# Optimization experiments

Measured on AMD Instinct MI355X. Metric: run time of the kernel, lower is better.

## Reference

```python
import jax, jax.numpy as jnp
import numpy as np

# dims (match init_kwargs / input_specs)
B, T, IN, H, OUT, BR = 128, 250, 700, 512, 20, 4
VTH, DT, WARMUP = 1.0, 1.0, 10


@jax.custom_vjp
def spike_fn(v):
    # Heaviside spike with surrogate gradient (ActFun_adp style)
    return (v > 0.0).astype(v.dtype)

def _spike_fwd(v):
    return spike_fn(v), v

def _spike_bwd(v, g):
    gamma, lens = 0.5, 0.5  # gaussian surrogate
    return (g * gamma * jnp.exp(-v * v / (2.0 * lens * lens)),)

spike_fn.defvjp(_spike_fwd, _spike_bwd)


def make_mask(rng, out_dim, in_dim, branch):
    # each output neuron's branch j sees a disjoint random slice of inputs
    m = np.zeros((out_dim * branch, in_dim), np.float32)
    seg = in_dim // branch
    for i in range(out_dim):
        perm = rng.permutation(in_dim)
        for j in range(branch):
            m[i * branch + j, perm[j * seg:(j + 1) * seg]] = 1.0
    return jnp.asarray(m)


def setup_inputs() -> dict:
    key = jax.random.key(0)
    ks = jax.random.split(key, 12)
    rng = np.random.default_rng(0)
    lim1 = 1.0 / np.sqrt(IN)
    lim2 = 1.0 / np.sqrt(H)
    return {
        "x": jax.random.uniform(ks[0], (B, T, IN), dtype=jnp.float32),
        "W1": jax.random.uniform(ks[1], (H * BR, IN), minval=-lim1, maxval=lim1),
        "b1": jax.random.uniform(ks[2], (H * BR,), minval=-lim1, maxval=lim1),
        "tau_m1": jax.random.uniform(ks[3], (H,), minval=0.0, maxval=4.0),
        "tau_n1": jax.random.uniform(ks[4], (H, BR), minval=0.0, maxval=4.0),
        "mask1": make_mask(rng, H, IN, BR),
        "W2": jax.random.uniform(ks[5], (H * BR, H), minval=-lim2, maxval=lim2),
        "b2": jax.random.uniform(ks[6], (H * BR,), minval=-lim2, maxval=lim2),
        "tau_m2": jax.random.uniform(ks[7], (H,), minval=0.0, maxval=4.0),
        "tau_n2": jax.random.uniform(ks[8], (H, BR), minval=0.0, maxval=4.0),
        "mask2": make_mask(rng, H, H, BR),
        "Wo": jax.random.uniform(ks[9], (OUT, H), minval=-lim2, maxval=lim2),
        "bo": jax.random.uniform(ks[10], (OUT,), minval=-lim2, maxval=lim2),
        "tau_mo": jax.random.uniform(ks[11], (OUT,), minval=0.0, maxval=4.0),
    }


def reference(x, W1, b1, tau_m1, tau_n1, mask1, W2, b2, tau_m2, tau_n2, mask2, Wo, bo, tau_mo):
    beta1 = jax.nn.sigmoid(tau_n1)   # [H,BR] dendritic decay
    alpha1 = jax.nn.sigmoid(tau_m1)  # [H]   membrane decay
    beta2 = jax.nn.sigmoid(tau_n2)
    alpha2 = jax.nn.sigmoid(tau_m2)
    alpha_o = jax.nn.sigmoid(tau_mo)  # [OUT]
    Wm1 = W1 * mask1  # dendritic branch connectivity mask
    Wm2 = W2 * mask2
    Bsz = x.shape[0]
    Hd, Br = tau_n1.shape
    Od = tau_mo.shape[0]

    init = (jnp.zeros((Bsz, Hd, Br)), jnp.zeros((Bsz, Hd)), jnp.zeros((Bsz, Hd)),
            jnp.zeros((Bsz, Hd, Br)), jnp.zeros((Bsz, Hd)), jnp.zeros((Bsz, Hd)),
            jnp.zeros((Bsz, Od)))

    def step(c, xt):
        d1, m1, s1, d2, m2, s2, mo = c
        # layer 1: dendritic filter then LIF membrane with soft reset
        d1 = beta1 * d1 + (1.0 - beta1) * (xt @ Wm1.T + b1).reshape(Bsz, Hd, Br)
        m1 = m1 * alpha1 + (1.0 - alpha1) * DT * d1.sum(-1) - VTH * s1
        s1 = spike_fn(m1 - VTH)
        # layer 2
        d2 = beta2 * d2 + (1.0 - beta2) * (s1 @ Wm2.T + b2).reshape(Bsz, Hd, Br)
        m2 = m2 * alpha2 + (1.0 - alpha2) * DT * d2.sum(-1) - VTH * s2
        s2 = spike_fn(m2 - VTH)
        # leaky readout integrator (no spiking)
        mo = mo * alpha_o + (1.0 - alpha_o) * DT * (s2 @ Wo.T + bo)
        return (d1, m1, s1, d2, m2, s2, mo), jax.nn.softmax(mo, axis=1)

    _, ys = jax.lax.scan(step, init, jnp.swapaxes(x, 0, 1))  # ys: [T,B,OUT]
    # readout_mode == 'sum_softmax': skip steps i <= warmup_steps, sum the rest
    return ys[WARMUP + 1:].sum(0)
```

## Files before the change

kernel.cpp:

```cpp
#include <hip/hip_runtime.h>
#include <math.h>
#include <stdint.h>

#define B_    128
#define T_    250
#define IN_   700
#define INP_  704
#define H_    512
#define OUT_  20
#define BR_   4
#define HB_   2048
#define WARM_ 10
#define VTH_  1.0f

typedef __attribute__((ext_vector_type(8)))  _Float16 half8;
typedef __attribute__((ext_vector_type(4)))  float f32x4;
typedef __attribute__((ext_vector_type(16))) float f32x16;
typedef __attribute__((ext_vector_type(4)))  int i32x4;
typedef __attribute__((ext_vector_type(16))) int i32x16;
typedef const __attribute__((address_space(1))) void* gptr_t;
typedef __attribute__((address_space(3))) void* lptr_t;

__global__ __launch_bounds__(256)
void w1prep_kernel(const float* __restrict__ W, const float* __restrict__ M,
                   _Float16* __restrict__ w0, _Float16* __restrict__ w1) {
    int i = blockIdx.x * 256 + threadIdx.x;
    if (i >= HB_ * INP_) return;
    int r = i / INP_, c = i - r * INP_;
    float v = (c < IN_) ? W[(size_t)r * IN_ + c] * M[(size_t)r * IN_ + c] : 0.f;
    _Float16 h0 = (_Float16)v;
    w0[i] = h0;
    w1[i] = (_Float16)(v - (float)h0);
}

__global__ __launch_bounds__(256)
void w2prep_kernel(const float* __restrict__ W, const float* __restrict__ M,
                   int8_t* __restrict__ p2, int8_t* __restrict__ p1,
                   int8_t* __restrict__ p0) {
    int i = blockIdx.x * 256 + threadIdx.x;
    if (i >= HB_ * H_) return;
    float v = W[i] * M[i];
    int q = (int)lrintf(v * 67108864.f);
    int b0 = (int)(int8_t)(q & 0xFF);  q = (q - b0) >> 8;
    int b1 = (int)(int8_t)(q & 0xFF);  int b2 = (q - b1) >> 8;
    p0[i] = (int8_t)b0; p1[i] = (int8_t)b1; p2[i] = (int8_t)b2;
}

__global__ __launch_bounds__(256)
void woprep_kernel(const float* __restrict__ Wo, _Float16* __restrict__ wo0,
                   _Float16* __restrict__ wo1) {
    int i = blockIdx.x * 256 + threadIdx.x;
    if (i >= 32 * H_) return;
    int n = i >> 9;
    float v = (n < OUT_) ? Wo[(size_t)n * H_ + (i & (H_ - 1))] : 0.f;
    _Float16 h0 = (_Float16)v;
    wo0[i] = h0;
    wo1[i] = (_Float16)(v - (float)h0);
}

__global__ __launch_bounds__(256)
void convx_kernel(const float* __restrict__ x, _Float16* __restrict__ x0,
                  _Float16* __restrict__ x1, int t0, int tc, int ntot) {
    int i = blockIdx.x * 256 + threadIdx.x;
    if (i >= ntot) return;
    int r = i / INP_, c = i - r * INP_;
    int bb = r / tc, tl = r - bb * tc;
    float v = (c < IN_) ? x[((size_t)bb * T_ + t0 + tl) * IN_ + c] : 0.f;
    _Float16 h0 = (_Float16)v;
    x0[i] = h0;
    x1[i] = (_Float16)(v - (float)h0);
}

__global__ void zero_kernel(float* __restrict__ p, int n4) {
    int i = blockIdx.x * blockDim.x + threadIdx.x;
    if (i < n4) ((float4*)p)[i] = make_float4(0.f, 0.f, 0.f, 0.f);
}

__global__ __launch_bounds__(256)
void l1_gemm_kernel(const _Float16* __restrict__ x0, const _Float16* __restrict__ x1,
                    const _Float16* __restrict__ w0, const _Float16* __restrict__ w1,
                    const float* __restrict__ bias, float* __restrict__ C) {
    __shared__ alignas(16) _Float16 A0s[128 * 32];
    __shared__ alignas(16) _Float16 A1s[128 * 32];
    __shared__ alignas(16) _Float16 B0s[128 * 32];
    __shared__ alignas(16) _Float16 B1s[128 * 32];
    const int tid  = threadIdx.x;
    const int wave = tid >> 6, lane = tid & 63;
    const int bm = blockIdx.y * 128, bn = blockIdx.x * 128;

    const int    srow  = tid >> 2;
    const int    skoff = (((tid & 3) ^ ((srow >> 1) & 3)) * 8);
    const size_t aoff0 = (size_t)(bm + srow) * INP_ + skoff;
    const size_t aoff1 = aoff0 + (size_t)64 * INP_;
    const size_t boff0 = (size_t)(bn + srow) * INP_ + skoff;
    const size_t boff1 = boff0 + (size_t)64 * INP_;
    const int lo0 = wave * 512, lo1 = 2048 + wave * 512;

    const int wm = wave & 1, wn = wave >> 1;
    const int row = lane & 31;
    const int khq = lane >> 5;
    const int key = (lane >> 1) & 3;
    const int cK0 = ((0 + khq) ^ key) * 8;
    const int cK1 = ((2 + khq) ^ key) * 8;

    f32x16 acc[2][2] = {};

    for (int kt = 0; kt < INP_ / 32; kt++) {
        const int k0 = kt * 32;
        __builtin_amdgcn_global_load_lds((gptr_t)(x0 + aoff0 + k0), (lptr_t)(A0s + lo0), 16, 0, 0);
        __builtin_amdgcn_global_load_lds((gptr_t)(x0 + aoff1 + k0), (lptr_t)(A0s + lo1), 16, 0, 0);
        __builtin_amdgcn_global_load_lds((gptr_t)(x1 + aoff0 + k0), (lptr_t)(A1s + lo0), 16, 0, 0);
        __builtin_amdgcn_global_load_lds((gptr_t)(x1 + aoff1 + k0), (lptr_t)(A1s + lo1), 16, 0, 0);
        __builtin_amdgcn_global_load_lds((gptr_t)(w0 + boff0 + k0), (lptr_t)(B0s + lo0), 16, 0, 0);
        __builtin_amdgcn_global_load_lds((gptr_t)(w0 + boff1 + k0), (lptr_t)(B0s + lo1), 16, 0, 0);
        __builtin_amdgcn_global_load_lds((gptr_t)(w1 + boff0 + k0), (lptr_t)(B1s + lo0), 16, 0, 0);
        __builtin_amdgcn_global_load_lds((gptr_t)(w1 + boff1 + k0), (lptr_t)(B1s + lo1), 16, 0, 0);
        __syncthreads();

        half8 a0f[2][2], a1f[2][2], b0f[2][2], b1f[2][2];
#pragma unroll
        for (int mt = 0; mt < 2; mt++) {
            const _Float16* ar = &A0s[(wm * 64 + mt * 32 + row) * 32];
            a0f[mt][0] = *(const half8*)&ar[cK0];
            a0f[mt][1] = *(const half8*)&ar[cK1];
        }
#pragma unroll
        for (int nt = 0; nt < 2; nt++) {
            const _Float16* br = &B0s[(wn * 64 + nt * 32 + row) * 32];
            b0f[nt][0] = *(const half8*)&br[cK0];
            b0f[nt][1] = *(const half8*)&br[cK1];
        }
#pragma unroll
        for (int ks = 0; ks < 2; ks++)
#pragma unroll
            for (int mt = 0; mt < 2; mt++)
#pragma unroll
                for (int nt = 0; nt < 2; nt++)
                    acc[mt][nt] = __builtin_amdgcn_mfma_f32_32x32x16_f16(
                        a0f[mt][ks], b0f[nt][ks], acc[mt][nt], 0, 0, 0);
#pragma unroll
        for (int nt = 0; nt < 2; nt++) {
            const _Float16* br = &B1s[(wn * 64 + nt * 32 + row) * 32];
            b1f[nt][0] = *(const half8*)&br[cK0];
            b1f[nt][1] = *(const half8*)&br[cK1];
        }
#pragma unroll
        for (int ks = 0; ks < 2; ks++)
#pragma unroll
            for (int mt = 0; mt < 2; mt++)
#pragma unroll
                for (int nt = 0; nt < 2; nt++)
                    acc[mt][nt] = __builtin_amdgcn_mfma_f32_32x32x16_f16(
                        a0f[mt][ks], b1f[nt][ks], acc[mt][nt], 0, 0, 0);
#pragma unroll
        for (int mt = 0; mt < 2; mt++) {
            const _Float16* ar = &A1s[(wm * 64 + mt * 32 + row) * 32];
            a1f[mt][0] = *(const half8*)&ar[cK0];
            a1f[mt][1] = *(const half8*)&ar[cK1];
        }
#pragma unroll
        for (int ks = 0; ks < 2; ks++)
#pragma unroll
            for (int mt = 0; mt < 2; mt++)
#pragma unroll
                for (int nt = 0; nt < 2; nt++)
                    acc[mt][nt] = __builtin_amdgcn_mfma_f32_32x32x16_f16(
                        a1f[mt][ks], b0f[nt][ks], acc[mt][nt], 0, 0, 0);
        __syncthreads();
    }

    const int col = lane & 31;
    const int rb  = 4 * (lane >> 5);
#pragma unroll
    for (int nt = 0; nt < 2; nt++) {
        const int gc = bn + wn * 64 + nt * 32 + col;
        const float bv = bias[gc];
#pragma unroll
        for (int mt = 0; mt < 2; mt++) {
#pragma unroll
            for (int reg = 0; reg < 16; reg++) {
                const int gr = bm + wm * 64 + mt * 32 + (reg & 3) + 8 * (reg >> 2) + rb;
                C[(size_t)gr * HB_ + gc] = acc[mt][nt][reg] + bv;
            }
        }
    }
}

__global__ __launch_bounds__(256)
void mfma_i8_gemm_kernel(const int8_t* __restrict__ A,
                         const int8_t* __restrict__ p2, const int8_t* __restrict__ p1,
                         const int8_t* __restrict__ p0,
                         const float* __restrict__ bias, float* __restrict__ C) {
    __shared__ alignas(16) int8_t As[128 * 64];
    __shared__ alignas(16) int8_t Bs[128 * 64];
    const int tid  = threadIdx.x;
    const int wave = tid >> 6, lane = tid & 63;
    const int bm = blockIdx.y * 128, bn = blockIdx.x * 128;

    const int    srow  = tid >> 2;
    const int    skoff = (((tid & 3) ^ ((srow >> 1) & 3)) * 16);
    const size_t aoff0 = (size_t)(bm + srow) * H_ + skoff;
    const size_t aoff1 = aoff0 + (size_t)64 * H_;
    const size_t boff0 = (size_t)(bn + srow) * H_ + skoff;
    const size_t boff1 = boff0 + (size_t)64 * H_;
    lptr_t lA0 = (lptr_t)(As + wave * 1024);
    lptr_t lA1 = (lptr_t)(As + 4096 + wave * 1024);
    lptr_t lB0 = (lptr_t)(Bs + wave * 1024);
    lptr_t lB1 = (lptr_t)(Bs + 4096 + wave * 1024);

    const int wm = wave & 1, wn = wave >> 1;
    const int row = lane & 31;
    const int khq = lane >> 5;
    const int key = (lane >> 1) & 3;
    const int cK0 = ((0 + khq) ^ key) * 16;
    const int cK1 = ((2 + khq) ^ key) * 16;

    const int8_t* planes[3] = {p2, p1, p0};
    i32x16 acc[2][2] = {};

#pragma unroll
    for (int s = 0; s < 3; s++) {
        if (s) {
#pragma unroll
            for (int mt = 0; mt < 2; mt++)
#pragma unroll
                for (int nt = 0; nt < 2; nt++) acc[mt][nt] *= 256;
        }
        const int8_t* pw = planes[s];
        for (int kt = 0; kt < H_ / 64; kt++) {
            const int k0 = kt * 64;
            __builtin_amdgcn_global_load_lds((gptr_t)(A  + aoff0 + k0), lA0, 16, 0, 0);
            __builtin_amdgcn_global_load_lds((gptr_t)(A  + aoff1 + k0), lA1, 16, 0, 0);
            __builtin_amdgcn_global_load_lds((gptr_t)(pw + boff0 + k0), lB0, 16, 0, 0);
            __builtin_amdgcn_global_load_lds((gptr_t)(pw + boff1 + k0), lB1, 16, 0, 0);
            __syncthreads();

            i32x4 af[2][2], bf[2][2];
#pragma unroll
            for (int mt = 0; mt < 2; mt++) {
                const int8_t* ar = &As[(wm * 64 + mt * 32 + row) * 64];
                af[mt][0] = *(const i32x4*)&ar[cK0];
                af[mt][1] = *(const i32x4*)&ar[cK1];
            }
#pragma unroll
            for (int nt = 0; nt < 2; nt++) {
                const int8_t* br = &Bs[(wn * 64 + nt * 32 + row) * 64];
                bf[nt][0] = *(const i32x4*)&br[cK0];
                bf[nt][1] = *(const i32x4*)&br[cK1];
            }
#pragma unroll
            for (int ks = 0; ks < 2; ks++)
#pragma unroll
                for (int mt = 0; mt < 2; mt++)
#pragma unroll
                    for (int nt = 0; nt < 2; nt++)
                        acc[mt][nt] = __builtin_amdgcn_mfma_i32_32x32x32_i8(
                            af[mt][ks], bf[nt][ks], acc[mt][nt], 0, 0, 0);
            __syncthreads();
        }
    }

    const float scale = 1.f / 67108864.f;
    const int col = lane & 31;
    const int rb  = 4 * (lane >> 5);
#pragma unroll
    for (int nt = 0; nt < 2; nt++) {
        const int gc = bn + wn * 64 + nt * 32 + col;
        const float bv = bias[gc];
#pragma unroll
        for (int mt = 0; mt < 2; mt++) {
#pragma unroll
            for (int reg = 0; reg < 16; reg++) {
                const int gr = bm + wm * 64 + mt * 32 + (reg & 3) + 8 * (reg >> 2) + rb;
                C[(size_t)gr * HB_ + gc] = (float)acc[mt][nt][reg] * scale + bv;
            }
        }
    }
}

#define SCAN_BODY(SPIKE_STORE)                                                  \
    int idx = blockIdx.x * 256 + threadIdx.x;                                   \
    int b = idx >> 9;                                                           \
    int h = idx & (H_ - 1);                                                     \
    float alpha = 1.f / (1.f + expf(-tau_m[h]));                                \
    float4 tn = ((const float4*)tau_n)[h];                                      \
    float4 beta;                                                                \
    beta.x = 1.f / (1.f + expf(-tn.x));                                         \
    beta.y = 1.f / (1.f + expf(-tn.y));                                         \
    beta.z = 1.f / (1.f + expf(-tn.z));                                         \
    beta.w = 1.f / (1.f + expf(-tn.w));                                         \
    float4 d = ((const float4*)dst)[idx];                                       \
    float m = mst[idx];                                                         \
    float sp = spst[idx];                                                       \
    const float* cp = cur + (size_t)b * tc * HB_ + h * BR_;                     \
    for (int t = 0; t < tc; t++) {                                              \
        float4 c = *(const float4*)cp;                                          \
        cp += HB_;                                                              \
        d.x = beta.x * d.x + (1.f - beta.x) * c.x;                              \
        d.y = beta.y * d.y + (1.f - beta.y) * c.y;                              \
        d.z = beta.z * d.z + (1.f - beta.z) * c.z;                              \
        d.w = beta.w * d.w + (1.f - beta.w) * c.w;                              \
        float s4 = ((d.x + d.y) + d.z) + d.w;                                   \
        m = m * alpha + (1.f - alpha) * s4 - VTH_ * sp;                         \
        sp = (m > VTH_) ? 1.f : 0.f;                                            \
        SPIKE_STORE;                                                            \
    }                                                                           \
    ((float4*)dst)[idx] = d;                                                    \
    mst[idx] = m;                                                               \
    spst[idx] = sp;

__global__ __launch_bounds__(256)
void scan_i8_kernel(const float* __restrict__ cur, float* __restrict__ dst,
                    float* __restrict__ mst, float* __restrict__ spst,
                    int8_t* __restrict__ sout, const float* __restrict__ tau_m,
                    const float* __restrict__ tau_n, int tc) {
    SCAN_BODY(sout[((size_t)b * tc + t) * H_ + h] = (int8_t)(m > VTH_))
}

__global__ __launch_bounds__(256)
void scan_f16_kernel(const float* __restrict__ cur, float* __restrict__ dst,
                     float* __restrict__ mst, float* __restrict__ spst,
                     _Float16* __restrict__ sout, const float* __restrict__ tau_m,
                     const float* __restrict__ tau_n, int tc) {
    SCAN_BODY(sout[((size_t)b * tc + t) * H_ + h] = (_Float16)sp)
}

__global__ __launch_bounds__(256)
void rdot_mfma_kernel(const _Float16* __restrict__ s2c, const _Float16* __restrict__ wo0,
                      const _Float16* __restrict__ wo1, const float* __restrict__ bo,
                      float* __restrict__ curo, int t0, int tc) {
    __shared__ alignas(16) _Float16 As[128 * 32];
    __shared__ alignas(16) _Float16 B0s[32 * 32];
    __shared__ alignas(16) _Float16 B1s[32 * 32];
    const int tid  = threadIdx.x;
    const int wave = tid >> 6, lane = tid & 63;
    const int bm = blockIdx.x * 128;

    const int    srow  = tid >> 2;
    const int    skoff = (((tid & 3) ^ ((srow >> 1) & 3)) * 8);
    const size_t aoff0 = (size_t)(bm + srow) * H_ + skoff;
    const size_t aoff1 = aoff0 + (size_t)64 * H_;
    lptr_t lA0 = (lptr_t)(As + wave * 512);
    lptr_t lA1 = (lptr_t)(As + 2048 + wave * 512);
    const _Float16* bsrc = (wave < 2) ? wo0 : wo1;
    const int bw = wave & 1;
    const size_t boff = (size_t)(bw * 16 + (lane >> 2)) * H_
                      + ((lane & 3) ^ ((lane >> 3) & 3)) * 8;
    lptr_t lB = (lptr_t)(((wave < 2) ? B0s : B1s) + bw * 512);

    const int fr = lane & 15;
    const int key = (lane >> 1) & 3;
    const int cK  = (((lane >> 4) ^ key) * 8);

    f32x4 acc[2][2] = {};

    for (int kt = 0; kt < H_ / 32; kt++) {
        const int k0 = kt * 32;
        __builtin_amdgcn_global_load_lds((gptr_t)(s2c + aoff0 + k0), lA0, 16, 0, 0);
        __builtin_amdgcn_global_load_lds((gptr_t)(s2c + aoff1 + k0), lA1, 16, 0, 0);
        __builtin_amdgcn_global_load_lds((gptr_t)(bsrc + boff + k0), lB, 16, 0, 0);
        __syncthreads();

        half8 af[2], b0[2], b1[2];
#pragma unroll
        for (int mi = 0; mi < 2; mi++)
            af[mi] = *(const half8*)&As[(wave * 32 + mi * 16 + fr) * 32 + cK];
#pragma unroll
        for (int ni = 0; ni < 2; ni++) {
            b0[ni] = *(const half8*)&B0s[(ni * 16 + fr) * 32 + cK];
            b1[ni] = *(const half8*)&B1s[(ni * 16 + fr) * 32 + cK];
        }
#pragma unroll
        for (int mi = 0; mi < 2; mi++)
#pragma unroll
            for (int ni = 0; ni < 2; ni++) {
                acc[mi][ni] = __builtin_amdgcn_mfma_f32_16x16x32_f16(af[mi], b0[ni], acc[mi][ni], 0, 0, 0);
                acc[mi][ni] = __builtin_amdgcn_mfma_f32_16x16x32_f16(af[mi], b1[ni], acc[mi][ni], 0, 0, 0);
            }
        __syncthreads();
    }

    const int cc = lane & 15;
    const int cr = (lane >> 4) * 4;
#pragma unroll
    for (int ni = 0; ni < 2; ni++) {
        const int gc = ni * 16 + cc;
        if (gc < OUT_) {
            const float bv = bo[gc];
#pragma unroll
            for (int mi = 0; mi < 2; mi++) {
#pragma unroll
                for (int r = 0; r < 4; r++) {
                    const int gr = bm + wave * 32 + mi * 16 + cr + r;
                    const int bb = gr / tc, tl = gr - bb * tc;
                    curo[((size_t)bb * T_ + t0 + tl) * OUT_ + gc] = acc[mi][ni][r] + bv;
                }
            }
        }
    }
}

#define RT_SEG 12
#define RT_LEN 21

__global__ __launch_bounds__(256)
void readout_kernel(const float* __restrict__ curo, const float* __restrict__ tau_mo,
                    float* __restrict__ out) {
    __shared__ float moS[T_ * OUT_];
    __shared__ float segA[RT_SEG][OUT_];
    __shared__ float segU[RT_SEG][OUT_];
    __shared__ float pre[RT_SEG][OUT_];
    __shared__ float accS[OUT_];
    const int b = blockIdx.x;
    const int tid = threadIdx.x;
    const float* cb = curo + (size_t)b * T_ * OUT_;

    const int o = tid % OUT_;
    const int sg = tid / OUT_;
    const float ao = 1.f / (1.f + expf(-tau_mo[o]));

    if (tid < RT_SEG * OUT_) {
        int t0 = sg * RT_LEN;
        int t1 = min(T_, t0 + RT_LEN);
        float u = 0.f, Ap = 1.f;
        for (int t = t0; t < t1; t++) {
            u = ao * u + (1.f - ao) * cb[t * OUT_ + o];
            Ap *= ao;
        }
        segU[sg][o] = u; segA[sg][o] = Ap;
    }
    if (tid < OUT_) accS[tid] = 0.f;
    __syncthreads();
    if (tid < OUT_) {
        float m = 0.f;
        for (int s = 0; s < RT_SEG; s++) {
            pre[s][tid] = m;
            m = segA[s][tid] * m + segU[s][tid];
        }
    }
    __syncthreads();
    if (tid < RT_SEG * OUT_) {
        int t0 = sg * RT_LEN;
        int t1 = min(T_, t0 + RT_LEN);
        float m = pre[sg][o];
        for (int t = t0; t < t1; t++) {
            m = ao * m + (1.f - ao) * cb[t * OUT_ + o];
            moS[t * OUT_ + o] = m;
        }
    }
    __syncthreads();
    if (tid >= WARM_ + 1 && tid < T_) {
        int t = tid;
        float mx = -3.0e38f;
#pragma unroll
        for (int o2 = 0; o2 < OUT_; o2++) mx = fmaxf(mx, moS[t * OUT_ + o2]);
        float es[OUT_]; float se = 0.f;
#pragma unroll
        for (int o2 = 0; o2 < OUT_; o2++) {
            float e = expf(moS[t * OUT_ + o2] - mx);
            es[o2] = e; se += e;
        }
        float inv = 1.f / se;
#pragma unroll
        for (int o2 = 0; o2 < OUT_; o2++) atomicAdd(&accS[o2], es[o2] * inv);
    }
    __syncthreads();
    if (tid < OUT_) out[(size_t)b * OUT_ + tid] = accS[tid];
}

extern "C" void kernel_launch(void* const* d_in, const int* in_sizes, int n_in,
                              void* d_out, int out_size, void* d_ws, size_t ws_size,
                              hipStream_t stream) {
    const float* x      = (const float*)d_in[0];
    const float* W1     = (const float*)d_in[1];
    const float* b1     = (const float*)d_in[2];
    const float* tau_m1 = (const float*)d_in[3];
    const float* tau_n1 = (const float*)d_in[4];
    const float* mask1  = (const float*)d_in[5];
    const float* W2     = (const float*)d_in[6];
    const float* b2     = (const float*)d_in[7];
    const float* tau_m2 = (const float*)d_in[8];
    const float* tau_n2 = (const float*)d_in[9];
    const float* mask2  = (const float*)d_in[10];
    const float* Wo     = (const float*)d_in[11];
    const float* bo     = (const float*)d_in[12];
    const float* tau_mo = (const float*)d_in[13];
    float* out = (float*)d_out;

    int ncs;  int tcs[3];
    bool single = (ws_size >= (size_t)368000000);
    if (single)                                { ncs = 1; tcs[0] = 250; }
    else if (ws_size >= (size_t)219000000)     { ncs = 2; tcs[0] = tcs[1] = 125; }
    else                                       { ncs = 3; tcs[0] = 100; tcs[1] = 100; tcs[2] = 50; }
    const int tcm = tcs[0];

    char* p = (char*)d_ws;
    auto alloc = [&](size_t bytes) { char* r = p; p += (bytes + 255) & ~(size_t)255; return r; };
    _Float16* w10 = (_Float16*)alloc((size_t)HB_ * INP_ * 2);
    _Float16* w11 = (_Float16*)alloc((size_t)HB_ * INP_ * 2);
    int8_t*   q2  = (int8_t*)alloc((size_t)HB_ * H_);
    int8_t*   q1  = (int8_t*)alloc((size_t)HB_ * H_);
    int8_t*   q0  = (int8_t*)alloc((size_t)HB_ * H_);
    _Float16* wo0 = (_Float16*)alloc((size_t)32 * H_ * 2);
    _Float16* wo1 = (_Float16*)alloc((size_t)32 * H_ * 2);
    _Float16* xc0 = (_Float16*)alloc((size_t)B_ * tcm * INP_ * 2);
    _Float16* xc1 = (_Float16*)alloc((size_t)B_ * tcm * INP_ * 2);
    int8_t*   s1c;
    _Float16* s2c;
    if (single) {
        s1c = (int8_t*)xc0;
        s2c = (_Float16*)xc1;
    } else {
        s1c = (int8_t*)alloc((size_t)B_ * tcm * H_);
        s2c = (_Float16*)alloc((size_t)B_ * tcm * H_ * 2);
    }
    float* cur    = (float*)alloc((size_t)B_ * tcm * HB_ * 4);
    float* curo   = (float*)alloc((size_t)B_ * T_ * OUT_ * 4);
    float* st     = (float*)alloc((size_t)786432 * 4);
    float* d1  = st;
    float* m1  = d1 + (size_t)B_ * H_ * BR_;
    float* sp1 = m1 + (size_t)B_ * H_;
    float* d2  = sp1 + (size_t)B_ * H_;
    float* m2  = d2 + (size_t)B_ * H_ * BR_;
    float* sp2 = m2 + (size_t)B_ * H_;

    w1prep_kernel<<<(HB_ * INP_ + 255) / 256, 256, 0, stream>>>(W1, mask1, w10, w11);
    w2prep_kernel<<<(HB_ * H_ + 255) / 256, 256, 0, stream>>>(W2, mask2, q2, q1, q0);
    woprep_kernel<<<(32 * H_ + 255) / 256, 256, 0, stream>>>(Wo, wo0, wo1);
    zero_kernel<<<(786432 / 4 + 255) / 256, 256, 0, stream>>>(st, 786432 / 4);

    int t0 = 0;
    for (int c = 0; c < ncs; c++) {
        const int tc = tcs[c];
        const int M = B_ * tc;
        dim3 gg(HB_ / 128, M / 128);
        convx_kernel<<<(M * INP_ + 255) / 256, 256, 0, stream>>>(x, xc0, xc1, t0, tc, M * INP_);
        l1_gemm_kernel<<<gg, 256, 0, stream>>>(xc0, xc1, w10, w11, b1, cur);
        scan_i8_kernel<<<B_ * H_ / 256, 256, 0, stream>>>(cur, d1, m1, sp1, s1c, tau_m1, tau_n1, tc);
        mfma_i8_gemm_kernel<<<gg, 256, 0, stream>>>(s1c, q2, q1, q0, b2, cur);
        scan_f16_kernel<<<B_ * H_ / 256, 256, 0, stream>>>(cur, d2, m2, sp2, s2c, tau_m2, tau_n2, tc);
        rdot_mfma_kernel<<<M / 128, 256, 0, stream>>>(s2c, wo0, wo1, bo, curo, t0, tc);
        t0 += tc;
    }
    readout_kernel<<<B_, 256, 0, stream>>>(curo, tau_mo, out);
}
```

Before: 826.3 us.

## Double-buffer LDS in GEMM kernels to overlap global loads with MFMA

Converts the layer-1 split-f16 GEMM, the int8 bit-plane GEMM and the readout MFMA kernel to double-buffered LDS staging. The next K tile is prefetched with global_load_lds while the current tile is computed, and one barrier per iteration replaces two. The int8 kernel's three plane loops are flattened into a single 24-step pipelined loop, with the accumulator rescaled at the plane boundaries. s_setprio is raised around the MFMA blocks. LDS use per block doubles, which may lower occupancy.

```diff
diff --git a/kernel.cpp b/kernel.cpp
--- a/kernel.cpp
+++ b/kernel.cpp
@@ -80,10 +80,7 @@
 void l1_gemm_kernel(const _Float16* __restrict__ x0, const _Float16* __restrict__ x1,
                     const _Float16* __restrict__ w0, const _Float16* __restrict__ w1,
                     const float* __restrict__ bias, float* __restrict__ C) {
-    __shared__ alignas(16) _Float16 A0s[128 * 32];
-    __shared__ alignas(16) _Float16 A1s[128 * 32];
-    __shared__ alignas(16) _Float16 B0s[128 * 32];
-    __shared__ alignas(16) _Float16 B1s[128 * 32];
+    __shared__ alignas(16) _Float16 S[2 * 16384];
     const int tid  = threadIdx.x;
     const int wave = tid >> 6, lane = tid & 63;
     const int bm = blockIdx.y * 128, bn = blockIdx.x * 128;
@@ -94,7 +91,7 @@
     const size_t aoff1 = aoff0 + (size_t)64 * INP_;
     const size_t boff0 = (size_t)(bn + srow) * INP_ + skoff;
     const size_t boff1 = boff0 + (size_t)64 * INP_;
-    const int lo0 = wave * 512, lo1 = 2048 + wave * 512;
+    const int lo = wave * 512;
 
     const int wm = wave & 1, wn = wave >> 1;
     const int row = lane & 31;
@@ -105,31 +102,38 @@
 
     f32x16 acc[2][2] = {};
 
-    for (int kt = 0; kt < INP_ / 32; kt++) {
+    auto stage = [&](int kt, int base) {
         const int k0 = kt * 32;
-        __builtin_amdgcn_global_load_lds((gptr_t)(x0 + aoff0 + k0), (lptr_t)(A0s + lo0), 16, 0, 0);
-        __builtin_amdgcn_global_load_lds((gptr_t)(x0 + aoff1 + k0), (lptr_t)(A0s + lo1), 16, 0, 0);
-        __builtin_amdgcn_global_load_lds((gptr_t)(x1 + aoff0 + k0), (lptr_t)(A1s + lo0), 16, 0, 0);
-        __builtin_amdgcn_global_load_lds((gptr_t)(x1 + aoff1 + k0), (lptr_t)(A1s + lo1), 16, 0, 0);
-        __builtin_amdgcn_global_load_lds((gptr_t)(w0 + boff0 + k0), (lptr_t)(B0s + lo0), 16, 0, 0);
-        __builtin_amdgcn_global_load_lds((gptr_t)(w0 + boff1 + k0), (lptr_t)(B0s + lo1), 16, 0, 0);
-        __builtin_amdgcn_global_load_lds((gptr_t)(w1 + boff0 + k0), (lptr_t)(B1s + lo0), 16, 0, 0);
-        __builtin_amdgcn_global_load_lds((gptr_t)(w1 + boff1 + k0), (lptr_t)(B1s + lo1), 16, 0, 0);
-        __syncthreads();
-
+        _Float16* Sb = S + base;
+        __builtin_amdgcn_global_load_lds((gptr_t)(x0 + aoff0 + k0), (lptr_t)(Sb + lo),          16, 0, 0);
+        __builtin_amdgcn_global_load_lds((gptr_t)(x0 + aoff1 + k0), (lptr_t)(Sb + 2048  + lo),  16, 0, 0);
+        __builtin_amdgcn_global_load_lds((gptr_t)(x1 + aoff0 + k0), (lptr_t)(Sb + 4096  + lo),  16, 0, 0);
+        __builtin_amdgcn_global_load_lds((gptr_t)(x1 + aoff1 + k0), (lptr_t)(Sb + 6144  + lo),  16, 0, 0);
+        __builtin_amdgcn_global_load_lds((gptr_t)(w0 + boff0 + k0), (lptr_t)(Sb + 8192  + lo),  16, 0, 0);
+        __builtin_amdgcn_global_load_lds((gptr_t)(w0 + boff1 + k0), (lptr_t)(Sb + 10240 + lo),  16, 0, 0);
+        __builtin_amdgcn_global_load_lds((gptr_t)(w1 + boff0 + k0), (lptr_t)(Sb + 12288 + lo),  16, 0, 0);
+        __builtin_amdgcn_global_load_lds((gptr_t)(w1 + boff1 + k0), (lptr_t)(Sb + 14336 + lo),  16, 0, 0);
+    };
+
+    auto compute = [&](int base) {
+        const _Float16* A0b = S + base;
+        const _Float16* A1b = A0b + 4096;
+        const _Float16* B0b = A0b + 8192;
+        const _Float16* B1b = A0b + 12288;
         half8 a0f[2][2], a1f[2][2], b0f[2][2], b1f[2][2];
 #pragma unroll
         for (int mt = 0; mt < 2; mt++) {
-            const _Float16* ar = &A0s[(wm * 64 + mt * 32 + row) * 32];
+            const _Float16* ar = &A0b[(wm * 64 + mt * 32 + row) * 32];
             a0f[mt][0] = *(const half8*)&ar[cK0];
             a0f[mt][1] = *(const half8*)&ar[cK1];
         }
 #pragma unroll
         for (int nt = 0; nt < 2; nt++) {
-            const _Float16* br = &B0s[(wn * 64 + nt * 32 + row) * 32];
+            const _Float16* br = &B0b[(wn * 64 + nt * 32 + row) * 32];
             b0f[nt][0] = *(const half8*)&br[cK0];
             b0f[nt][1] = *(const half8*)&br[cK1];
         }
+        __builtin_amdgcn_s_setprio(1);
 #pragma unroll
         for (int ks = 0; ks < 2; ks++)
 #pragma unroll
@@ -138,12 +142,14 @@
                 for (int nt = 0; nt < 2; nt++)
                     acc[mt][nt] = __builtin_amdgcn_mfma_f32_32x32x16_f16(
                         a0f[mt][ks], b0f[nt][ks], acc[mt][nt], 0, 0, 0);
+        __builtin_amdgcn_s_setprio(0);
 #pragma unroll
         for (int nt = 0; nt < 2; nt++) {
-            const _Float16* br = &B1s[(wn * 64 + nt * 32 + row) * 32];
+            const _Float16* br = &B1b[(wn * 64 + nt * 32 + row) * 32];
             b1f[nt][0] = *(const half8*)&br[cK0];
             b1f[nt][1] = *(const half8*)&br[cK1];
         }
+        __builtin_amdgcn_s_setprio(1);
 #pragma unroll
         for (int ks = 0; ks < 2; ks++)
 #pragma unroll
@@ -152,12 +158,14 @@
                 for (int nt = 0; nt < 2; nt++)
                     acc[mt][nt] = __builtin_amdgcn_mfma_f32_32x32x16_f16(
                         a0f[mt][ks], b1f[nt][ks], acc[mt][nt], 0, 0, 0);
+        __builtin_amdgcn_s_setprio(0);
 #pragma unroll
         for (int mt = 0; mt < 2; mt++) {
-            const _Float16* ar = &A1s[(wm * 64 + mt * 32 + row) * 32];
+            const _Float16* ar = &A1b[(wm * 64 + mt * 32 + row) * 32];
             a1f[mt][0] = *(const half8*)&ar[cK0];
             a1f[mt][1] = *(const half8*)&ar[cK1];
         }
+        __builtin_amdgcn_s_setprio(1);
 #pragma unroll
         for (int ks = 0; ks < 2; ks++)
 #pragma unroll
@@ -166,8 +174,23 @@
                 for (int nt = 0; nt < 2; nt++)
                     acc[mt][nt] = __builtin_amdgcn_mfma_f32_32x32x16_f16(
                         a1f[mt][ks], b0f[nt][ks], acc[mt][nt], 0, 0, 0);
-        __syncthreads();
-    }
+        __builtin_amdgcn_s_setprio(0);
+    };
+
+    stage(0, 0);
+    asm volatile("s_waitcnt vmcnt(0)" ::: "memory");
+    __builtin_amdgcn_s_barrier();
+
+    int cur = 0;
+    for (int kt = 0; kt < INP_ / 32 - 1; kt++) {
+        const int base = cur * 16384;
+        stage(kt + 1, base ^ 16384);
+        compute(base);
+        asm volatile("s_waitcnt vmcnt(0) lgkmcnt(0)" ::: "memory");
+        __builtin_amdgcn_s_barrier();
+        cur ^= 1;
+    }
+    compute(cur * 16384);
 
     const int col = lane & 31;
     const int rb  = 4 * (lane >> 5);
@@ -191,8 +214,7 @@
                          const int8_t* __restrict__ p2, const int8_t* __restrict__ p1,
                          const int8_t* __restrict__ p0,
                          const float* __restrict__ bias, float* __restrict__ C) {
-    __shared__ alignas(16) int8_t As[128 * 64];
-    __shared__ alignas(16) int8_t Bs[128 * 64];
+    __shared__ alignas(16) int8_t S[2 * 16384];
     const int tid  = threadIdx.x;
     const int wave = tid >> 6, lane = tid & 63;
     const int bm = blockIdx.y * 128, bn = blockIdx.x * 128;
@@ -203,10 +225,7 @@
     const size_t aoff1 = aoff0 + (size_t)64 * H_;
     const size_t boff0 = (size_t)(bn + srow) * H_ + skoff;
     const size_t boff1 = boff0 + (size_t)64 * H_;
-    lptr_t lA0 = (lptr_t)(As + wave * 1024);
-    lptr_t lA1 = (lptr_t)(As + 4096 + wave * 1024);
-    lptr_t lB0 = (lptr_t)(Bs + wave * 1024);
-    lptr_t lB1 = (lptr_t)(Bs + 4096 + wave * 1024);
+    const int lo = wave * 1024;
 
     const int wm = wave & 1, wn = wave >> 1;
     const int row = lane & 31;
@@ -215,50 +234,67 @@
     const int cK0 = ((0 + khq) ^ key) * 16;
     const int cK1 = ((2 + khq) ^ key) * 16;
 
-    const int8_t* planes[3] = {p2, p1, p0};
     i32x16 acc[2][2] = {};
 
-#pragma unroll
-    for (int s = 0; s < 3; s++) {
-        if (s) {
+    auto stage = [&](int i, int base) {
+        const int s  = i >> 3;
+        const int k0 = (i & 7) * 64;
+        const int8_t* pw = (s == 0) ? p2 : (s == 1) ? p1 : p0;
+        int8_t* Sb = S + base;
+        __builtin_amdgcn_global_load_lds((gptr_t)(A  + aoff0 + k0), (lptr_t)(Sb + lo),          16, 0, 0);
+        __builtin_amdgcn_global_load_lds((gptr_t)(A  + aoff1 + k0), (lptr_t)(Sb + 4096  + lo),  16, 0, 0);
+        __builtin_amdgcn_global_load_lds((gptr_t)(pw + boff0 + k0), (lptr_t)(Sb + 8192  + lo),  16, 0, 0);
+        __builtin_amdgcn_global_load_lds((gptr_t)(pw + boff1 + k0), (lptr_t)(Sb + 12288 + lo),  16, 0, 0);
+    };
+
+    auto compute = [&](int base) {
+        const int8_t* Ab = S + base;
+        const int8_t* Bb = Ab + 8192;
+        i32x4 af[2][2], bf[2][2];
+#pragma unroll
+        for (int mt = 0; mt < 2; mt++) {
+            const int8_t* ar = &Ab[(wm * 64 + mt * 32 + row) * 64];
+            af[mt][0] = *(const i32x4*)&ar[cK0];
+            af[mt][1] = *(const i32x4*)&ar[cK1];
+        }
+#pragma unroll
+        for (int nt = 0; nt < 2; nt++) {
+            const int8_t* br = &Bb[(wn * 64 + nt * 32 + row) * 64];
+            bf[nt][0] = *(const i32x4*)&br[cK0];
+            bf[nt][1] = *(const i32x4*)&br[cK1];
+        }
+        __builtin_amdgcn_s_setprio(1);
+#pragma unroll
+        for (int ks = 0; ks < 2; ks++)
 #pragma unroll
             for (int mt = 0; mt < 2; mt++)
 #pragma unroll
+                for (int nt = 0; nt < 2; nt++)
+                    acc[mt][nt] = __builtin_amdgcn_mfma_i32_32x32x32_i8(
+                        af[mt][ks], bf[nt][ks], acc[mt][nt], 0, 0, 0);
+        __builtin_amdgcn_s_setprio(0);
+    };
+
+    stage(0, 0);
+    asm volatile("s_waitcnt vmcnt(0)" ::: "memory");
+    __builtin_amdgcn_s_barrier();
+
+    int cur = 0;
+    for (int i = 0; i < 23; i++) {
+        const int base = cur * 16384;
+        stage(i + 1, base ^ 16384);
+        if (i == 8 || i == 16) {
+#pragma unroll
+            for (int mt = 0; mt < 2; mt++)
+#pragma unroll
                 for (int nt = 0; nt < 2; nt++) acc[mt][nt] *= 256;
         }
-        const int8_t* pw = planes[s];
-        for (int kt = 0; kt < H_ / 64; kt++) {
-            const int k0 = kt * 64;
-            __builtin_amdgcn_global_load_lds((gptr_t)(A  + aoff0 + k0), lA0, 16, 0, 0);
-            __builtin_amdgcn_global_load_lds((gptr_t)(A  + aoff1 + k0), lA1, 16, 0, 0);
-            __builtin_amdgcn_global_load_lds((gptr_t)(pw + boff0 + k0), lB0, 16, 0, 0);
-            __builtin_amdgcn_global_load_lds((gptr_t)(pw + boff1 + k0), lB1, 16, 0, 0);
-            __syncthreads();
-
-            i32x4 af[2][2], bf[2][2];
-#pragma unroll
-            for (int mt = 0; mt < 2; mt++) {
-                const int8_t* ar = &As[(wm * 64 + mt * 32 + row) * 64];
-                af[mt][0] = *(const i32x4*)&ar[cK0];
-                af[mt][1] = *(const i32x4*)&ar[cK1];
-            }
-#pragma unroll
-            for (int nt = 0; nt < 2; nt++) {
-                const int8_t* br = &Bs[(wn * 64 + nt * 32 + row) * 64];
-                bf[nt][0] = *(const i32x4*)&br[cK0];
-                bf[nt][1] = *(const i32x4*)&br[cK1];
-            }
-#pragma unroll
-            for (int ks = 0; ks < 2; ks++)
-#pragma unroll
-                for (int mt = 0; mt < 2; mt++)
-#pragma unroll
-                    for (int nt = 0; nt < 2; nt++)
-                        acc[mt][nt] = __builtin_amdgcn_mfma_i32_32x32x32_i8(
-                            af[mt][ks], bf[nt][ks], acc[mt][nt], 0, 0, 0);
-            __syncthreads();
-        }
-    }
+        compute(base);
+        asm volatile("s_waitcnt vmcnt(0) lgkmcnt(0)" ::: "memory");
+        __builtin_amdgcn_s_barrier();
+        cur ^= 1;
+    }
+    compute(cur * 16384);
 
     const float scale = 1.f / 67108864.f;
     const int col = lane & 31;
@@ -329,9 +365,7 @@
 void rdot_mfma_kernel(const _Float16* __restrict__ s2c, const _Float16* __restrict__ wo0,
                       const _Float16* __restrict__ wo1, const float* __restrict__ bo,
                       float* __restrict__ curo, int t0, int tc) {
-    __shared__ alignas(16) _Float16 As[128 * 32];
-    __shared__ alignas(16) _Float16 B0s[32 * 32];
-    __shared__ alignas(16) _Float16 B1s[32 * 32];
+    __shared__ alignas(16) _Float16 S[2 * 6144];
     const int tid  = threadIdx.x;
     const int wave = tid >> 6, lane = tid & 63;
     const int bm = blockIdx.x * 128;
@@ -340,13 +374,12 @@
     const int    skoff = (((tid & 3) ^ ((srow >> 1) & 3)) * 8);
     const size_t aoff0 = (size_t)(bm + srow) * H_ + skoff;
     const size_t aoff1 = aoff0 + (size_t)64 * H_;
-    lptr_t lA0 = (lptr_t)(As + wave * 512);
-    lptr_t lA1 = (lptr_t)(As + 2048 + wave * 512);
     const _Float16* bsrc = (wave < 2) ? wo0 : wo1;
     const int bw = wave & 1;
     const size_t boff = (size_t)(bw * 16 + (lane >> 2)) * H_
                       + ((lane & 3) ^ ((lane >> 3) & 3)) * 8;
-    lptr_t lB = (lptr_t)(((wave < 2) ? B0s : B1s) + bw * 512);
+    const int loA = wave * 512;
+    const int loB = 4096 + (wave >> 1) * 1024 + bw * 512;
 
     const int fr = lane & 15;
     const int key = (lane >> 1) & 3;
@@ -354,22 +387,28 @@
 
     f32x4 acc[2][2] = {};
 
-    for (int kt = 0; kt < H_ / 32; kt++) {
+    auto stage = [&](int kt, int base) {
         const int k0 = kt * 32;
-        __builtin_amdgcn_global_load_lds((gptr_t)(s2c + aoff0 + k0), lA0, 16, 0, 0);
-        __builtin_amdgcn_global_load_lds((gptr_t)(s2c + aoff1 + k0), lA1, 16, 0, 0);
-        __builtin_amdgcn_global_load_lds((gptr_t)(bsrc + boff + k0), lB, 16, 0, 0);
-        __syncthreads();
-
+        _Float16* Sb = S + base;
+        __builtin_amdgcn_global_load_lds((gptr_t)(s2c + aoff0 + k0),  (lptr_t)(Sb + loA),        16, 0, 0);
+        __builtin_amdgcn_global_load_lds((gptr_t)(s2c + aoff1 + k0),  (lptr_t)(Sb + 2048 + loA), 16, 0, 0);
+        __builtin_amdgcn_global_load_lds((gptr_t)(bsrc + boff + k0),  (lptr_t)(Sb + loB),        16, 0, 0);
+    };
+
+    auto compute = [&](int base) {
+        const _Float16* Ab  = S + base;
+        const _Float16* B0b = Ab + 4096;
+        const _Float16* B1b = Ab + 5120;
         half8 af[2], b0[2], b1[2];
 #pragma unroll
         for (int mi = 0; mi < 2; mi++)
-            af[mi] = *(const half8*)&As[(wave * 32 + mi * 16 + fr) * 32 + cK];
+            af[mi] = *(const half8*)&Ab[(wave * 32 + mi * 16 + fr) * 32 + cK];
 #pragma unroll
         for (int ni = 0; ni < 2; ni++) {
-            b0[ni] = *(const half8*)&B0s[(ni * 16 + fr) * 32 + cK];
-            b1[ni] = *(const half8*)&B1s[(ni * 16 + fr) * 32 + cK];
-        }
+            b0[ni] = *(const half8*)&B0b[(ni * 16 + fr) * 32 + cK];
+            b1[ni] = *(const half8*)&B1b[(ni * 16 + fr) * 32 + cK];
+        }
+        __builtin_amdgcn_s_setprio(1);
 #pragma unroll
         for (int mi = 0; mi < 2; mi++)
 #pragma unroll
@@ -377,8 +416,23 @@
                 acc[mi][ni] = __builtin_amdgcn_mfma_f32_16x16x32_f16(af[mi], b0[ni], acc[mi][ni], 0, 0, 0);
                 acc[mi][ni] = __builtin_amdgcn_mfma_f32_16x16x32_f16(af[mi], b1[ni], acc[mi][ni], 0, 0, 0);
             }
-        __syncthreads();
-    }
+        __builtin_amdgcn_s_setprio(0);
+    };
+
+    stage(0, 0);
+    asm volatile("s_waitcnt vmcnt(0)" ::: "memory");
+    __builtin_amdgcn_s_barrier();
+
+    int cur = 0;
+    for (int kt = 0; kt < H_ / 32 - 1; kt++) {
+        const int base = cur * 6144;
+        stage(kt + 1, base ^ 6144);
+        compute(base);
+        asm volatile("s_waitcnt vmcnt(0) lgkmcnt(0)" ::: "memory");
+        __builtin_amdgcn_s_barrier();
+        cur ^= 1;
+    }
+    compute(cur * 6144);
 
     const int cc = lane & 15;
     const int cr = (lane >> 4) * 4;
```

After: 827.7 us. Within noise of the previous version (+0.2%).
